# Kernel optimization log

Measured on AMD Instinct MI355X. Metric: run time of the kernel, lower is better.

The kernel has to match this reference:

```python
import jax, jax.numpy as jnp
import numpy as np

B = 65536          # graphs (agents)
NODES_PER = 9      # 1 torso + 8 joints
N = B * NODES_PER
D = 64
SOFTPLUS_BIAS = float(np.log(np.expm1(1.0)))  # biased_softplus_1.0 from NormalParamExtractor


def _star_edges():
    # bidirectional torso<->joint star per 9-node graph
    base = np.arange(B, dtype=np.int64) * NODES_PER          # torso ids [B]
    torso = np.repeat(base, 8)                               # [8B]
    joint = (base[:, None] + np.arange(1, 9, dtype=np.int64)[None, :]).reshape(-1)  # [8B]
    src = np.concatenate([torso, joint])                     # torso->joint, joint->torso
    dst = np.concatenate([joint, torso])
    return jnp.asarray(np.stack([src, dst], axis=0))         # [2, 16B]


def setup_inputs() -> dict:
    key = jax.random.key(0)
    ks = jax.random.split(key, 12)
    s = lambda fan_in: 1.0 / np.sqrt(fan_in)
    inp = {
        "x": jax.random.normal(ks[0], (N, 11), dtype=jnp.float32),
        "edge_index": _star_edges(),
        # input projections
        "W_joint": jax.random.uniform(ks[1], (2, D), jnp.float32, -s(2), s(2)),
        "b_joint": jnp.zeros((D,), jnp.float32),
        "W_torso": jax.random.uniform(ks[2], (11, D), jnp.float32, -s(11), s(11)),
        "b_torso": jnp.zeros((D,), jnp.float32),
        # GraphConv 1: lin_rel (bias) on aggregated neighbors + lin_root (no bias)
        "W_rel1": jax.random.uniform(ks[3], (D, D), jnp.float32, -s(D), s(D)),
        "b_rel1": jnp.zeros((D,), jnp.float32),
        "W_root1": jax.random.uniform(ks[4], (D, D), jnp.float32, -s(D), s(D)),
        # GraphConv 2
        "W_rel2": jax.random.uniform(ks[5], (D, D), jnp.float32, -s(D), s(D)),
        "b_rel2": jnp.zeros((D,), jnp.float32),
        "W_root2": jax.random.uniform(ks[6], (D, D), jnp.float32, -s(D), s(D)),
        # 8 per-joint heads Linear(64, 2)
        "W_heads": jax.random.uniform(ks[7], (8, D, 2), jnp.float32, -s(D), s(D)),
        "b_heads": jnp.zeros((8, 2), jnp.float32),
    }
    return inp


def _graph_conv(h, src, dst, W_rel, b_rel, W_root, n):
    # GraphConv (aggr='add'): out[i] = lin_rel(sum_{j->i} h[j]) + lin_root(h[i])
    agg = jax.ops.segment_sum(h[src], dst, num_segments=n)   # [N, D]
    return agg @ W_rel + b_rel + h @ W_root


def reference(x, edge_index, W_joint, b_joint, W_torso, b_torso,
              W_rel1, b_rel1, W_root1, W_rel2, b_rel2, W_root2,
              W_heads, b_heads):
    n = x.shape[0]
    b = n // NODES_PER
    xg = x.reshape(b, NODES_PER, 11)
    h_torso = xg[:, :1, :] @ W_torso + b_torso              # [b, 1, D]  (node 0 of each graph)
    h_joint = xg[:, 1:, :2] @ W_joint + b_joint             # [b, 8, D]
    h = jnp.concatenate([h_torso, h_joint], axis=1).reshape(n, D)
    src, dst = edge_index[0], edge_index[1]
    h = jnp.tanh(_graph_conv(h, src, dst, W_rel1, b_rel1, W_root1, n))
    h = jnp.tanh(_graph_conv(h, src, dst, W_rel2, b_rel2, W_root2, n))
    joints = h.reshape(b, NODES_PER, D)[:, 1:, :]           # [b, 8, D]
    out = jnp.einsum('bjd,jdo->bjo', joints, W_heads) + b_heads  # [b, 8, 2]
    loc = out[..., 0]                                       # [b, 8]
    scale = jax.nn.softplus(out[..., 1] + SOFTPLUS_BIAS)    # biased_softplus_1.0
    return loc, scale
```

## Files before the change

kernel.cpp:

```cpp
#include <hip/hip_runtime.h>


typedef __attribute__((ext_vector_type(8))) short bf16x8;
typedef __attribute__((ext_vector_type(4))) float f32x4;

#define SOFTPLUS_BIAS 0.5413248546129181f

#define LDS_H   0
#define LDS_S   18432
#define LDS_HW  20480
#define LDS_W   22528
#define LDS_SZ  38912

__device__ __forceinline__ unsigned int cvtpk(float lo, float hi) {
  unsigned int r;
  asm("v_cvt_pk_bf16_f32 %0, %1, %2" : "=v"(r) : "v"(lo), "v"(hi));
  return r;
}
__device__ __forceinline__ float asf(unsigned int u) {
  union { unsigned int i; float f; } v; v.i = u; return v.f;
}
__device__ __forceinline__ unsigned short f2bf(float f) {
  union { float f; unsigned int i; } v; v.f = f;
  unsigned int lsb = (v.i >> 16) & 1u;
  return (unsigned short)((v.i + 0x7fffu + lsb) >> 16);
}
__device__ __forceinline__ float fast_tanh(float x) {
  float e = __expf(2.0f * x);
  return 1.0f - 2.0f * __builtin_amdgcn_rcpf(e + 1.0f);
}

__global__ void pack_weights(const float* __restrict__ Wrel1, const float* __restrict__ Wroot1,
                             const float* __restrict__ Wrel2, const float* __restrict__ Wroot2,
                             const float* __restrict__ Wheads, unsigned short* __restrict__ ws) {
  int id = blockIdx.x * 256 + threadIdx.x;
  if (id < 16384) {
    const float* W = (id < 4096) ? Wrel1 : (id < 8192) ? Wroot1 : (id < 12288) ? Wrel2 : Wroot2;
    int m = id & 4095;
    int e = m & 7, lane = (m >> 3) & 63, nt = (m >> 9) & 3, ks = m >> 11;
    int k = ((lane >> 4) << 3) + e + (ks << 5);
    int col = (nt << 4) + (lane & 15);
    ws[id] = f2bf(W[k * 64 + col]);
  } else if (id < 17408) {
    int m = id - 16384;
    int e = m & 7, lane = (m >> 3) & 63, ks = m >> 9;
    int k = ((lane >> 4) << 3) + e + (ks << 5);
    int c = lane & 15, j = c >> 1, o = c & 1;
    ws[id] = f2bf(Wheads[(j * 64 + k) * 2 + o]);
  }
}

__launch_bounds__(256, 4)
__global__ void actor_main(const float* __restrict__ x,
                           const float* __restrict__ Wj_g, const float* __restrict__ bj_g,
                           const float* __restrict__ Wt_g, const float* __restrict__ bt_g,
                           const float* __restrict__ brel1_g, const float* __restrict__ brel2_g,
                           const float* __restrict__ bh_g,
                           const unsigned short* __restrict__ wsw,
                           float* __restrict__ out) {
  __shared__ __align__(16) unsigned char smem[LDS_SZ];
  const int t = threadIdx.x;
  const int lane = t & 63;
  const int w = t >> 6;
  const int gbase = blockIdx.x << 4;
  const int l15 = lane & 15;
  const int q = lane >> 4;
  const int ks16 = q << 4;
  const int relc = l15 + (w << 4);

  unsigned int aggA[9];
#pragma unroll
  for (int m = 0; m < 9; m++) {
    int r = (m << 4) + l15;
    int g = (57 * r) >> 9;
    int node = r - 9 * g;
    int row = (node == 0) ? g : 9 * g;
    unsigned int base = (node == 0) ? (unsigned)LDS_S : 0u;
    aggA[m] = base + row * 128 + (ks16 ^ ((row & 7) << 4));
  }
  const unsigned int h0b = l15 * 128 + (ks16 ^ ((l15 & 7) << 4));
  unsigned int wb[4];
#pragma unroll
  for (int i = 0; i < 4; i++) {
    int rr = (q << 2) + i;
    wb[i] = rr * 128 + ((2 * relc) ^ ((rr & 7) << 4));
  }

  {
    const float4* xg = reinterpret_cast<const float4*>(x + (size_t)gbase * 99);
    float4* xl4 = reinterpret_cast<float4*>(smem + LDS_W);
    xl4[t] = xg[t];
    if (t + 256 < 396) xl4[t + 256] = xg[t + 256];
    const bf16x8* hsrc = reinterpret_cast<const bf16x8*>(wsw + 16384);
    bf16x8* hdst = reinterpret_cast<bf16x8*>(smem + LDS_HW);
    if (t < 128) hdst[t] = hsrc[t];
  }
  float Wtr[11];
#pragma unroll
  for (int k = 0; k < 11; k++) Wtr[k] = Wt_g[k * 64 + lane];
  const float btr = bt_g[lane];
  const float Wj0 = Wj_g[lane], Wj1 = Wj_g[64 + lane], bjr = bj_g[lane];
  const float brelA = brel1_g[relc], brelB = brel2_g[relc];
  __syncthreads();

  const float* xl = reinterpret_cast<const float*>(smem + LDS_W);
#pragma unroll
  for (int it = 0; it < 4; it++) {
    int g = w + (it << 2);
    float acc1 = btr;
#pragma unroll
    for (int k = 0; k < 11; k++) acc1 += xl[g * 99 + k] * Wtr[k];
    int row = 9 * g;
    *reinterpret_cast<unsigned short*>(smem + row * 128 + ((2 * lane) ^ ((row & 7) << 4))) =
        (unsigned short)cvtpk(acc1, acc1);
  }
#pragma unroll
  for (int it = 0; it < 32; it++) {
    int jr = w + (it << 2);
    int g = jr >> 3, j = jr & 7;
    int xb = g * 99 + 11 + 11 * j;
    float acc1 = bjr + xl[xb] * Wj0 + xl[xb + 1] * Wj1;
    int row = 9 * g + 1 + j;
    *reinterpret_cast<unsigned short*>(smem + row * 128 + ((2 * lane) ^ ((row & 7) << 4))) =
        (unsigned short)cvtpk(acc1, acc1);
  }
  __syncthreads();

  {
    const bf16x8* wsrc = reinterpret_cast<const bf16x8*>(wsw);
    bf16x8* wdst = reinterpret_cast<bf16x8*>(smem + LDS_W);
#pragma unroll
    for (int i = 0; i < 4; i++) wdst[t + 256 * i] = wsrc[t + 256 * i];
  }

  f32x4 acc[9];
#pragma unroll
  for (int layer = 0; layer < 2; layer++) {
    const float brel = (layer == 0) ? brelA : brelB;

    {
      int gS = t >> 4, dq = t & 15;
      int rb = dq << 3;
      float s0 = 0.f, s1 = 0.f, s2 = 0.f, s3 = 0.f;
#pragma unroll
      for (int j = 0; j < 8; j++) {
        int row = 9 * gS + 1 + j;
        uint2 p = *reinterpret_cast<const uint2*>(smem + row * 128 + (rb ^ ((row & 7) << 4)));
        s0 += asf(p.x << 16); s1 += asf(p.x & 0xffff0000u);
        s2 += asf(p.y << 16); s3 += asf(p.y & 0xffff0000u);
      }
      uint2 o; o.x = cvtpk(s0, s1); o.y = cvtpk(s2, s3);
      *reinterpret_cast<uint2*>(smem + LDS_S + gS * 128 + (rb ^ ((gS & 7) << 4))) = o;
    }
    __syncthreads();

    const unsigned char* wrel = smem + LDS_W;
    const unsigned char* wroot = smem + LDS_W + 8192;
    bf16x8 bRel0  = *reinterpret_cast<const bf16x8*>(wrel  + ((0 + w) * 64 + lane) * 16);
    bf16x8 bRel1  = *reinterpret_cast<const bf16x8*>(wrel  + ((4 + w) * 64 + lane) * 16);
    bf16x8 bRoot0 = *reinterpret_cast<const bf16x8*>(wroot + ((0 + w) * 64 + lane) * 16);
    bf16x8 bRoot1 = *reinterpret_cast<const bf16x8*>(wroot + ((4 + w) * 64 + lane) * 16);

#pragma unroll
    for (int m = 0; m < 9; m++) {
      const int off = m * 2048;
      bf16x8 ag0 = *reinterpret_cast<const bf16x8*>(smem + aggA[m]);
      bf16x8 ag1 = *reinterpret_cast<const bf16x8*>(smem + (aggA[m] ^ 64u));
      bf16x8 a0  = *reinterpret_cast<const bf16x8*>(smem + h0b + off);
      bf16x8 a1  = *reinterpret_cast<const bf16x8*>(smem + (h0b ^ 64u) + off);
      f32x4 c = {brel, brel, brel, brel};
      c = __builtin_amdgcn_mfma_f32_16x16x32_bf16(ag0, bRel0, c, 0, 0, 0);
      c = __builtin_amdgcn_mfma_f32_16x16x32_bf16(ag1, bRel1, c, 0, 0, 0);
      c = __builtin_amdgcn_mfma_f32_16x16x32_bf16(a0, bRoot0, c, 0, 0, 0);
      acc[m] = __builtin_amdgcn_mfma_f32_16x16x32_bf16(a1, bRoot1, c, 0, 0, 0);
    }
    __syncthreads();

    if (layer == 0) {
      const bf16x8* wsrc2 = reinterpret_cast<const bf16x8*>(wsw + 8192);
      bf16x8* wdst = reinterpret_cast<bf16x8*>(smem + LDS_W);
#pragma unroll
      for (int i = 0; i < 4; i++) wdst[t + 256 * i] = wsrc2[t + 256 * i];
    }

#pragma unroll
    for (int m = 0; m < 9; m++) {
      const int off = m * 2048;
      float t0 = fast_tanh(acc[m][0]);
      float t1 = fast_tanh(acc[m][1]);
      float t2 = fast_tanh(acc[m][2]);
      float t3 = fast_tanh(acc[m][3]);
      unsigned int p0 = cvtpk(t0, t1);
      unsigned int p1 = cvtpk(t2, t3);
      *reinterpret_cast<unsigned short*>(smem + wb[0] + off) = (unsigned short)p0;
      *reinterpret_cast<unsigned short*>(smem + wb[1] + off) = (unsigned short)(p0 >> 16);
      *reinterpret_cast<unsigned short*>(smem + wb[2] + off) = (unsigned short)p1;
      *reinterpret_cast<unsigned short*>(smem + wb[3] + off) = (unsigned short)(p1 >> 16);
    }
    __syncthreads();
  }

  {
    const unsigned char* hw = smem + LDS_HW;
    bf16x8 hb0 = *reinterpret_cast<const bf16x8*>(hw + lane * 16);
    bf16x8 hb1 = *reinterpret_cast<const bf16x8*>(hw + (64 + lane) * 16);
    int c = l15;
#pragma unroll
    for (int u = 0; u < 2; u++) {
      int tt = (w << 1) + u;
      int jr = (tt << 4) + l15;
      int arow = 9 * (jr >> 3) + 1 + (jr & 7);
      unsigned int ha = arow * 128 + (ks16 ^ ((arow & 7) << 4));
      bf16x8 a0 = *reinterpret_cast<const bf16x8*>(smem + ha);
      bf16x8 a1 = *reinterpret_cast<const bf16x8*>(smem + (ha ^ 64u));
      f32x4 z = {0.f, 0.f, 0.f, 0.f};
      z = __builtin_amdgcn_mfma_f32_16x16x32_bf16(a0, hb0, z, 0, 0, 0);
      z = __builtin_amdgcn_mfma_f32_16x16x32_bf16(a1, hb1, z, 0, 0, 0);
#pragma unroll
      for (int i = 0; i < 4; i++) {
        int r = (tt << 4) + (q << 2) + i;
        int gg = r >> 3, j2 = r & 7;
        if (c == 2 * j2) {
          out[(size_t)(gbase + gg) * 8 + j2] = z[i] + bh_g[2 * j2];
        } else if (c == 2 * j2 + 1) {
          float zz = z[i] + bh_g[2 * j2 + 1] + SOFTPLUS_BIAS;
          float sp = (zz > 20.0f) ? zz : __logf(1.0f + __expf(zz));
          out[524288 + (size_t)(gbase + gg) * 8 + j2] = sp;
        }
      }
    }
  }
}

extern "C" void kernel_launch(void* const* d_in, const int* in_sizes, int n_in,
                              void* d_out, int out_size, void* d_ws, size_t ws_size,
                              hipStream_t stream) {
  const float* x      = (const float*)d_in[0];
  const float* Wj     = (const float*)d_in[2];
  const float* bj     = (const float*)d_in[3];
  const float* Wt     = (const float*)d_in[4];
  const float* bt     = (const float*)d_in[5];
  const float* Wrel1  = (const float*)d_in[6];
  const float* brel1  = (const float*)d_in[7];
  const float* Wroot1 = (const float*)d_in[8];
  const float* Wrel2  = (const float*)d_in[9];
  const float* brel2  = (const float*)d_in[10];
  const float* Wroot2 = (const float*)d_in[11];
  const float* Wheads = (const float*)d_in[12];
  const float* bh     = (const float*)d_in[13];
  unsigned short* ws16 = (unsigned short*)d_ws;
  float* out = (float*)d_out;

  hipLaunchKernelGGL(pack_weights, dim3(68), dim3(256), 0, stream,
                     Wrel1, Wroot1, Wrel2, Wroot2, Wheads, ws16);
  hipLaunchKernelGGL(actor_main, dim3(4096), dim3(256), 0, stream,
                     x, Wj, bj, Wt, bt, brel1, brel2, bh, ws16, out);
}
```

Measured before the change: 69.84 us.

## Load MFMA weight fragments from global directly, shrinking LDS for higher occupancy

```diff
diff --git a/kernel.cpp b/kernel.cpp
--- a/kernel.cpp
+++ b/kernel.cpp
@@ -8,9 +8,8 @@
 
 #define LDS_H   0
 #define LDS_S   18432
-#define LDS_HW  20480
-#define LDS_W   22528
-#define LDS_SZ  38912
+#define LDS_X   20480
+#define LDS_SZ  26816
 
 __device__ __forceinline__ unsigned int cvtpk(float lo, float hi) {
   unsigned int r;
@@ -50,7 +49,7 @@
   }
 }
 
-__launch_bounds__(256, 4)
+__launch_bounds__(256, 6)
 __global__ void actor_main(const float* __restrict__ x,
                            const float* __restrict__ Wj_g, const float* __restrict__ bj_g,
                            const float* __restrict__ Wt_g, const float* __restrict__ bt_g,
@@ -68,6 +67,8 @@
   const int ks16 = q << 4;
   const int relc = l15 + (w << 4);
 
+  const bf16x8* wsv = reinterpret_cast<const bf16x8*>(wsw);
+
   unsigned int aggA[9];
 #pragma unroll
   for (int m = 0; m < 9; m++) {
@@ -78,22 +79,19 @@
     unsigned int base = (node == 0) ? (unsigned)LDS_S : 0u;
     aggA[m] = base + row * 128 + (ks16 ^ ((row & 7) << 4));
   }
-  const unsigned int h0b = l15 * 128 + (ks16 ^ ((l15 & 7) << 4));
+  const unsigned int h0b = l15 * 128 + (unsigned)(ks16 ^ ((l15 & 7) << 4));
   unsigned int wb[4];
 #pragma unroll
   for (int i = 0; i < 4; i++) {
     int rr = (q << 2) + i;
-    wb[i] = rr * 128 + ((2 * relc) ^ ((rr & 7) << 4));
+    wb[i] = rr * 128 + (unsigned)((2 * relc) ^ ((rr & 7) << 4));
   }
 
   {
     const float4* xg = reinterpret_cast<const float4*>(x + (size_t)gbase * 99);
-    float4* xl4 = reinterpret_cast<float4*>(smem + LDS_W);
+    float4* xl4 = reinterpret_cast<float4*>(smem + LDS_X);
     xl4[t] = xg[t];
     if (t + 256 < 396) xl4[t + 256] = xg[t + 256];
-    const bf16x8* hsrc = reinterpret_cast<const bf16x8*>(wsw + 16384);
-    bf16x8* hdst = reinterpret_cast<bf16x8*>(smem + LDS_HW);
-    if (t < 128) hdst[t] = hsrc[t];
   }
   float Wtr[11];
 #pragma unroll
@@ -103,7 +101,7 @@
   const float brelA = brel1_g[relc], brelB = brel2_g[relc];
   __syncthreads();
 
-  const float* xl = reinterpret_cast<const float*>(smem + LDS_W);
+  const float* xl = reinterpret_cast<const float*>(smem + LDS_X);
 #pragma unroll
   for (int it = 0; it < 4; it++) {
     int g = w + (it << 2);
@@ -126,17 +124,15 @@
   }
   __syncthreads();
 
-  {
-    const bf16x8* wsrc = reinterpret_cast<const bf16x8*>(wsw);
-    bf16x8* wdst = reinterpret_cast<bf16x8*>(smem + LDS_W);
-#pragma unroll
-    for (int i = 0; i < 4; i++) wdst[t + 256 * i] = wsrc[t + 256 * i];
-  }
-
   f32x4 acc[9];
 #pragma unroll
   for (int layer = 0; layer < 2; layer++) {
-    const float brel = (layer == 0) ? brelA : brelB;
+    const int lbase = layer ? 1024 : 0;
+    bf16x8 bRel0  = wsv[lbase + (0 + w) * 64 + lane];
+    bf16x8 bRel1  = wsv[lbase + (4 + w) * 64 + lane];
+    bf16x8 bRoot0 = wsv[lbase + 512 + (0 + w) * 64 + lane];
+    bf16x8 bRoot1 = wsv[lbase + 512 + (4 + w) * 64 + lane];
+    const float brel = layer ? brelB : brelA;
 
     {
       int gS = t >> 4, dq = t & 15;
@@ -154,20 +150,12 @@
     }
     __syncthreads();
 
-    const unsigned char* wrel = smem + LDS_W;
-    const unsigned char* wroot = smem + LDS_W + 8192;
-    bf16x8 bRel0  = *reinterpret_cast<const bf16x8*>(wrel  + ((0 + w) * 64 + lane) * 16);
-    bf16x8 bRel1  = *reinterpret_cast<const bf16x8*>(wrel  + ((4 + w) * 64 + lane) * 16);
-    bf16x8 bRoot0 = *reinterpret_cast<const bf16x8*>(wroot + ((0 + w) * 64 + lane) * 16);
-    bf16x8 bRoot1 = *reinterpret_cast<const bf16x8*>(wroot + ((4 + w) * 64 + lane) * 16);
-
 #pragma unroll
     for (int m = 0; m < 9; m++) {
-      const int off = m * 2048;
       bf16x8 ag0 = *reinterpret_cast<const bf16x8*>(smem + aggA[m]);
       bf16x8 ag1 = *reinterpret_cast<const bf16x8*>(smem + (aggA[m] ^ 64u));
-      bf16x8 a0  = *reinterpret_cast<const bf16x8*>(smem + h0b + off);
-      bf16x8 a1  = *reinterpret_cast<const bf16x8*>(smem + (h0b ^ 64u) + off);
+      bf16x8 a0  = *reinterpret_cast<const bf16x8*>(smem + h0b + m * 2048);
+      bf16x8 a1  = *reinterpret_cast<const bf16x8*>(smem + (h0b ^ 64u) + m * 2048);
       f32x4 c = {brel, brel, brel, brel};
       c = __builtin_amdgcn_mfma_f32_16x16x32_bf16(ag0, bRel0, c, 0, 0, 0);
       c = __builtin_amdgcn_mfma_f32_16x16x32_bf16(ag1, bRel1, c, 0, 0, 0);
@@ -176,22 +164,11 @@
     }
     __syncthreads();
 
-    if (layer == 0) {
-      const bf16x8* wsrc2 = reinterpret_cast<const bf16x8*>(wsw + 8192);
-      bf16x8* wdst = reinterpret_cast<bf16x8*>(smem + LDS_W);
-#pragma unroll
-      for (int i = 0; i < 4; i++) wdst[t + 256 * i] = wsrc2[t + 256 * i];
-    }
-
 #pragma unroll
     for (int m = 0; m < 9; m++) {
       const int off = m * 2048;
-      float t0 = fast_tanh(acc[m][0]);
-      float t1 = fast_tanh(acc[m][1]);
-      float t2 = fast_tanh(acc[m][2]);
-      float t3 = fast_tanh(acc[m][3]);
-      unsigned int p0 = cvtpk(t0, t1);
-      unsigned int p1 = cvtpk(t2, t3);
+      unsigned p0 = cvtpk(fast_tanh(acc[m][0]), fast_tanh(acc[m][1]));
+      unsigned p1 = cvtpk(fast_tanh(acc[m][2]), fast_tanh(acc[m][3]));
       *reinterpret_cast<unsigned short*>(smem + wb[0] + off) = (unsigned short)p0;
       *reinterpret_cast<unsigned short*>(smem + wb[1] + off) = (unsigned short)(p0 >> 16);
       *reinterpret_cast<unsigned short*>(smem + wb[2] + off) = (unsigned short)p1;
@@ -201,16 +178,15 @@
   }
 
   {
-    const unsigned char* hw = smem + LDS_HW;
-    bf16x8 hb0 = *reinterpret_cast<const bf16x8*>(hw + lane * 16);
-    bf16x8 hb1 = *reinterpret_cast<const bf16x8*>(hw + (64 + lane) * 16);
+    bf16x8 hb0 = wsv[2048 + lane];
+    bf16x8 hb1 = wsv[2048 + 64 + lane];
     int c = l15;
 #pragma unroll
     for (int u = 0; u < 2; u++) {
       int tt = (w << 1) + u;
       int jr = (tt << 4) + l15;
       int arow = 9 * (jr >> 3) + 1 + (jr & 7);
-      unsigned int ha = arow * 128 + (ks16 ^ ((arow & 7) << 4));
+      unsigned ha = arow * 128 + (unsigned)(ks16 ^ ((arow & 7) << 4));
       bf16x8 a0 = *reinterpret_cast<const bf16x8*>(smem + ha);
       bf16x8 a1 = *reinterpret_cast<const bf16x8*>(smem + (ha ^ 64u));
       f32x4 z = {0.f, 0.f, 0.f, 0.f};
```

New measurement: 86.46 us. 23.8% more time.
